# Performance work log

Measured on AMD Instinct MI355X. Metric: run time of the kernel, lower is better.

## Reference

```python
import jax, jax.numpy as jnp
import numpy as np

B, N, D = 2, 2048, 1024
H = 16
DH = D // H
WINDOW = 64
SCALE = 1.0 / np.sqrt(DH).astype(np.float32)


def setup_inputs() -> dict:
    key = jax.random.key(0)
    k1, k2, k3 = jax.random.split(key, 3)
    # xavier-uniform-like scales for the projections
    lim_qkv = np.sqrt(6.0 / (D + 3 * D)).astype(np.float32)
    lim_out = np.sqrt(6.0 / (D + D)).astype(np.float32)
    x = jax.random.normal(k1, (B, N, D), dtype=jnp.float32)
    Wqkv = jax.random.uniform(k2, (3 * D, D), dtype=jnp.float32, minval=-lim_qkv, maxval=lim_qkv)
    bqkv = jnp.zeros((3 * D,), dtype=jnp.float32)
    Wout = jax.random.uniform(k3, (D, D), dtype=jnp.float32, minval=-lim_out, maxval=lim_out)
    bout = jnp.zeros((D,), dtype=jnp.float32)
    return {"x": x, "Wqkv": Wqkv, "bqkv": bqkv, "Wout": Wout, "bout": bout}


def _causal_window_mask(n: int) -> jnp.ndarray:
    pos = jnp.arange(n)
    diff = pos[:, None] - pos[None, :]  # query_pos - key_pos
    return (diff >= 0) & (diff < WINDOW)  # [N, N] bool


def reference(x, Wqkv, bqkv, Wout, bout):
    b, n, d = x.shape
    qkv = x @ Wqkv.T + bqkv                      # [B, N, 3D]
    qkv = qkv.reshape(b, n, 3, H, DH)
    qkv = jnp.transpose(qkv, (2, 0, 3, 1, 4))    # [3, B, H, N, DH]
    q, k, v = qkv[0], qkv[1], qkv[2]
    scores = jnp.einsum('bhqd,bhkd->bhqk', q, k) * SCALE  # [B, H, N, N]
    mask = _causal_window_mask(n)
    neg_inf = jnp.asarray(-jnp.inf, dtype=scores.dtype)
    scores = jnp.where(mask[None, None], scores, neg_inf)
    attn = jax.nn.softmax(scores, axis=-1)
    out = jnp.einsum('bhqk,bhkd->bhqd', attn, v)  # [B, H, N, DH]
    out = jnp.transpose(out, (0, 2, 1, 3)).reshape(b, n, d)
    return out @ Wout.T + bout
```

## Files before the change

### kernel.cpp

```cpp
#include <hip/hip_runtime.h>
#include <hip/hip_bf16.h>


typedef __attribute__((ext_vector_type(8))) __bf16 bf16x8;
typedef __attribute__((ext_vector_type(4))) float f32x4;

#define GLOAD16(g, l)                                              \
  __builtin_amdgcn_global_load_lds(                                \
      (const __attribute__((address_space(1))) void*)(g),          \
      (__attribute__((address_space(3))) void*)(l), 16, 0, 0)

#define MFMA16(a, b, c) __builtin_amdgcn_mfma_f32_16x16x32_bf16((a), (b), (c), 0, 0, 0)

__global__ __launch_bounds__(256) void cvt3(const float* __restrict__ x,
                                            const float* __restrict__ wqkv,
                                            const float* __restrict__ wout,
                                            __bf16* __restrict__ xb,
                                            __bf16* __restrict__ wqkvb,
                                            __bf16* __restrict__ woutb) {
  const int blk = blockIdx.x;
  const float* src;
  __bf16* dst;
  int i;
  if (blk < 2048) {
    src = x; dst = xb; i = (blk * 256 + (int)threadIdx.x) * 8;
  } else if (blk < 3584) {
    src = wqkv; dst = wqkvb; i = ((blk - 2048) * 256 + (int)threadIdx.x) * 8;
  } else {
    src = wout; dst = woutb; i = ((blk - 3584) * 256 + (int)threadIdx.x) * 8;
  }
  f32x4 a = *(const f32x4*)(src + i);
  f32x4 b = *(const f32x4*)(src + i + 4);
  bf16x8 o;
  o[0] = (__bf16)a[0]; o[1] = (__bf16)a[1]; o[2] = (__bf16)a[2]; o[3] = (__bf16)a[3];
  o[4] = (__bf16)b[0]; o[5] = (__bf16)b[1]; o[6] = (__bf16)b[2]; o[7] = (__bf16)b[3];
  *(bf16x8*)(dst + i) = o;
}

template <int MODE, int WM>
__global__ __launch_bounds__(WM * 128) void gemm_ct(
    const __bf16* __restrict__ A, const __bf16* __restrict__ Bw,
    const float* __restrict__ bias, int N,
    float* __restrict__ outF,
    __bf16* __restrict__ qo, __bf16* __restrict__ ko, __bf16* __restrict__ vt,
    int nbn, int chunk) {
  constexpr int K = 1024;
  constexpr int ASZ = WM * 8192;
  constexpr int BUF = ASZ + 16384;
  __shared__ __align__(16) unsigned char Ls[2 * BUF];
  const int tid = threadIdx.x;
  const int lane = tid & 63;
  const int wid = tid >> 6;
  const int wr = (WM == 2) ? (wid >> 1) : 0;
  const int wc = (WM == 2) ? (wid & 1) : wid;
  const int colL = lane & 15, g = lane >> 4;

  int s = (int)blockIdx.x;
  s = (s & 7) * chunk + (s >> 3);
  const int m0 = (s / nbn) * (WM * 64), n0 = (s % nbn) * 128;

  const __bf16* Ap = A + (size_t)m0 * K;
  const __bf16* Bp = Bw + (size_t)n0 * K;

  auto stageA = [&](unsigned char* lds, int k0) {
#pragma unroll
    for (int it = 0; it < 4; ++it) {
      int c = tid + it * (WM * 128);
      int row = c >> 3, p = c & 7, q = p ^ (row & 7);
      GLOAD16(Ap + (size_t)row * K + k0 + (q << 3), lds + c * 16);
    }
  };
  auto stageB = [&](unsigned char* lds, int k0) {
#pragma unroll
    for (int it = 0; it < 8 / WM; ++it) {
      int c = tid + it * (WM * 128);
      int row = c >> 3, p = c & 7, q = p ^ (row & 7);
      GLOAD16(Bp + (size_t)row * K + k0 + (q << 3), lds + c * 16);
    }
  };

  f32x4 acc[4][4] = {};

  stageA(Ls, 0);
  stageB(Ls + ASZ, 0);
  stageA(Ls + BUF, 64);
  stageB(Ls + BUF + ASZ, 64);
  if constexpr (WM == 2) asm volatile("s_waitcnt vmcnt(8)" ::: "memory");
  else                   asm volatile("s_waitcnt vmcnt(12)" ::: "memory");
  __builtin_amdgcn_s_barrier();

  constexpr int nT = 16;
  for (int t = 0; t < nT; ++t) {
    const unsigned char* Ab = Ls + (t & 1) * BUF;
    const unsigned char* Bb = Ab + ASZ;
    bf16x8 af[4][2], bf[4][2];
#pragma unroll
    for (int mi = 0; mi < 4; ++mi) {
      const int r = (wr << 6) + (mi << 4) + colL;
#pragma unroll
      for (int kk = 0; kk < 2; ++kk)
        af[mi][kk] = *(const bf16x8*)(Ab + r * 128 + ((((kk << 2) + g) ^ (r & 7)) << 4));
    }
#pragma unroll
    for (int ni = 0; ni < 4; ++ni) {
      const int r = (wc << 6) + (ni << 4) + colL;
#pragma unroll
      for (int kk = 0; kk < 2; ++kk)
        bf[ni][kk] = *(const bf16x8*)(Bb + r * 128 + ((((kk << 2) + g) ^ (r & 7)) << 4));
    }
#pragma unroll
    for (int mi = 0; mi < 4; ++mi)
#pragma unroll
      for (int ni = 0; ni < 4; ++ni) {
        acc[mi][ni] = MFMA16(af[mi][0], bf[ni][0], acc[mi][ni]);
        acc[mi][ni] = MFMA16(af[mi][1], bf[ni][1], acc[mi][ni]);
      }
    asm volatile("s_waitcnt lgkmcnt(0)" ::: "memory");
    __builtin_amdgcn_s_barrier();
    if (t < nT - 2) {
      const int kn = (t + 2) << 6;
      unsigned char* dst = Ls + (t & 1) * BUF;
      stageA(dst, kn);
      stageB(dst + ASZ, kn);
      if constexpr (WM == 2) asm volatile("s_waitcnt vmcnt(8)" ::: "memory");
      else                   asm volatile("s_waitcnt vmcnt(12)" ::: "memory");
    } else {
      asm volatile("s_waitcnt vmcnt(0)" ::: "memory");
    }
    __builtin_amdgcn_s_barrier();
  }

  if (MODE == 0) {
    const int Cn0 = n0 + (wc << 6);
    const int sx = Cn0 >> 10, h = (Cn0 >> 6) & 15;
    float bv[4];
#pragma unroll
    for (int ni = 0; ni < 4; ++ni) bv[ni] = bias[Cn0 + (ni << 4) + colL];
    const int b = m0 >> 11;
    if (sx == 2) {
      unsigned char* wreg = Ls + wid * 9216;
#pragma unroll
      for (int mi = 0; mi < 4; ++mi)
#pragma unroll
        for (int ni = 0; ni < 4; ++ni)
#pragma unroll
          for (int jp = 0; jp < 2; ++jp) {
            const int tt = (mi << 4) + (g << 2) + (jp << 1);
            const int d = (ni << 4) + colL;
            unsigned short u0 = __builtin_bit_cast(
                unsigned short, (__bf16)(acc[mi][ni][jp * 2] + bv[ni]));
            unsigned short u1 = __builtin_bit_cast(
                unsigned short, (__bf16)(acc[mi][ni][jp * 2 + 1] + bv[ni]));
            *(unsigned int*)(wreg + ((d * 72 + tt) << 1)) =
                (unsigned int)u0 | ((unsigned int)u1 << 16);
          }
      asm volatile("s_waitcnt lgkmcnt(0)" ::: "memory");
      const size_t vbase = (size_t)(b * 16 + h) * 64 * 2048;
      const int tg0 = (m0 & 2047) + (wr << 6);
#pragma unroll
      for (int i = 0; i < 32; ++i) {
        const int d = (i << 1) + (lane >> 5);
        const int toff = (lane & 31) << 1;
        unsigned int v = *(unsigned int*)(wreg + (d * 144 + ((lane & 31) << 2)));
        *(unsigned int*)((unsigned short*)vt + vbase + (size_t)d * 2048 + tg0 + toff) = v;
      }
    } else {
      __bf16* dst = (sx == 0) ? qo : ko;
      const float mul = (sx == 0) ? 0.125f : 1.0f;
#pragma unroll
      for (int mi = 0; mi < 4; ++mi) {
#pragma unroll
        for (int j = 0; j < 4; ++j) {
          const int Rm = m0 + (wr << 6) + (mi << 4) + (g << 2) + j;
          const int tt = Rm & 2047;
          __bf16* rowp = dst + (((size_t)b * 16 + h) * 2048 + tt) * 64;
#pragma unroll
          for (int ni = 0; ni < 4; ++ni)
            rowp[(ni << 4) + colL] = (__bf16)((acc[mi][ni][j] + bv[ni]) * mul);
        }
      }
    }
  } else {
    float bv[4];
#pragma unroll
    for (int ni = 0; ni < 4; ++ni) bv[ni] = bias[n0 + (wc << 6) + (ni << 4) + colL];
#pragma unroll
    for (int mi = 0; mi < 4; ++mi) {
#pragma unroll
      for (int j = 0; j < 4; ++j) {
        const int Rm = m0 + (wr << 6) + (mi << 4) + (g << 2) + j;
        float* rowp = outF + (size_t)Rm * N + n0 + (wc << 6);
#pragma unroll
        for (int ni = 0; ni < 4; ++ni)
          rowp[(ni << 4) + colL] = acc[mi][ni][j] + bv[ni];
      }
    }
  }
}

__global__ __launch_bounds__(256) void attn_win(const __bf16* __restrict__ Qb,
                                                const __bf16* __restrict__ Kb,
                                                const __bf16* __restrict__ Vt,
                                                __bf16* __restrict__ Ob) {
  const int bh = blockIdx.x >> 5;
  const int qb = blockIdx.x & 31;
  const int b = bh >> 4, h = bh & 15;
  __shared__ __align__(16) unsigned char Qs[64 * 128];
  __shared__ __align__(16) unsigned char Ks[128 * 128];
  __shared__ __align__(16) unsigned char Vs[64 * 256];
  __shared__ __align__(16) unsigned char Ps[4 * 16 * 272];
  const int tid = threadIdx.x;
  const int lane = tid & 63;
  const int w = tid >> 6;
  const int colL = lane & 15, g = lane >> 4;
  const __bf16* Qg = Qb + (size_t)bh * 2048 * 64;
  const __bf16* Kg = Kb + (size_t)bh * 2048 * 64;
  const __bf16* Vg = Vt + (size_t)bh * 64 * 2048;
  const int t0 = qb * 64 - 64;

#pragma unroll
  for (int it = 0; it < 2; ++it) {
    int c = tid + (it << 8);
    int r = c >> 3, p = c & 7, q = p ^ (r & 7);
    GLOAD16(Qg + (size_t)(qb * 64 + r) * 64 + (q << 3), Qs + c * 16);
  }
#pragma unroll
  for (int it = 0; it < 4; ++it) {
    int c = tid + (it << 8);
    int r = c >> 3, p = c & 7, q = p ^ (r & 7);
    int tok = t0 + r;
    tok = tok < 0 ? 0 : tok;
    GLOAD16(Kg + (size_t)tok * 64 + (q << 3), Ks + c * 16);
  }
#pragma unroll
  for (int it = 0; it < 4; ++it) {
    int c = tid + (it << 8);
    int r = c >> 4, p = c & 15, q = p ^ (r & 7);
    int tk = t0 + (q << 3);
    tk = tk < 0 ? 0 : tk;
    GLOAD16(Vg + (size_t)r * 2048 + tk, Vs + c * 16);
  }
  __syncthreads();

  f32x4 sc[8] = {};
  bf16x8 qf[2];
#pragma unroll
  for (int kk = 0; kk < 2; ++kk) {
    int r = (w << 4) + colL;
    int slot = (kk << 2) + g;
    qf[kk] = *(const bf16x8*)(Qs + r * 128 + ((slot ^ (r & 7)) << 4));
  }
#pragma unroll
  for (int ni = 0; ni < 8; ++ni) {
#pragma unroll
    for (int kk = 0; kk < 2; ++kk) {
      int r = (ni << 4) + colL;
      int slot = (kk << 2) + g;
      bf16x8 kf = *(const bf16x8*)(Ks + r * 128 + ((slot ^ (r & 7)) << 4));
      sc[ni] = MFMA16(qf[kk], kf, sc[ni]);
    }
  }

  float mx[4], sm[4];
#pragma unroll
  for (int j = 0; j < 4; ++j) mx[j] = -3.0e38f;
#pragma unroll
  for (int ni = 0; ni < 8; ++ni) {
#pragma unroll
    for (int j = 0; j < 4; ++j) {
      const int qi = (w << 4) + (g << 2) + j;
      const int ki = (ni << 4) + colL;
      const bool valid = (ki > qi) && (ki <= qi + 64) && (qb > 0 || ki >= 64);
      if (!valid) sc[ni][j] = -3.0e38f;
      mx[j] = fmaxf(mx[j], sc[ni][j]);
    }
  }
#pragma unroll
  for (int j = 0; j < 4; ++j) {
    mx[j] = fmaxf(mx[j], __shfl_xor(mx[j], 1));
    mx[j] = fmaxf(mx[j], __shfl_xor(mx[j], 2));
    mx[j] = fmaxf(mx[j], __shfl_xor(mx[j], 4));
    mx[j] = fmaxf(mx[j], __shfl_xor(mx[j], 8));
    sm[j] = 0.0f;
  }
  unsigned char* ps = Ps + w * (16 * 272);
#pragma unroll
  for (int ni = 0; ni < 8; ++ni) {
#pragma unroll
    for (int j = 0; j < 4; ++j) {
      float p = __expf(sc[ni][j] - mx[j]);
      sm[j] += p;
      *(__bf16*)(ps + ((g << 2) + j) * 272 + (((ni << 4) + colL) << 1)) = (__bf16)p;
    }
  }
#pragma unroll
  for (int j = 0; j < 4; ++j) {
    sm[j] += __shfl_xor(sm[j], 1);
    sm[j] += __shfl_xor(sm[j], 2);
    sm[j] += __shfl_xor(sm[j], 4);
    sm[j] += __shfl_xor(sm[j], 8);
  }
  __syncthreads();

  f32x4 o[4] = {};
#pragma unroll
  for (int step = 0; step < 4; ++step) {
    bf16x8 pf = *(const bf16x8*)(ps + colL * 272 + (step << 6) + (g << 4));
#pragma unroll
    for (int dt = 0; dt < 4; ++dt) {
      int r = (dt << 4) + colL;
      int slot = (step << 2) + g;
      bf16x8 vf = *(const bf16x8*)(Vs + r * 256 + ((slot ^ (r & 7)) << 4));
      o[dt] = MFMA16(pf, vf, o[dt]);
    }
  }

  float rinv[4];
#pragma unroll
  for (int j = 0; j < 4; ++j) rinv[j] = 1.0f / sm[j];
#pragma unroll
  for (int dt = 0; dt < 4; ++dt) {
#pragma unroll
    for (int j = 0; j < 4; ++j) {
      const int t = qb * 64 + (w << 4) + (g << 2) + j;
      Ob[((size_t)b * 2048 + t) * 1024 + h * 64 + (dt << 4) + colL] =
          (__bf16)(o[dt][j] * rinv[j]);
    }
  }
}

extern "C" void kernel_launch(void* const* d_in, const int* in_sizes, int n_in,
                              void* d_out, int out_size, void* d_ws, size_t ws_size,
                              hipStream_t stream) {
  const float* x = (const float*)d_in[0];
  const float* Wqkv = (const float*)d_in[1];
  const float* bqkv = (const float*)d_in[2];
  const float* Wout = (const float*)d_in[3];
  const float* bout = (const float*)d_in[4];
  float* out = (float*)d_out;

  __bf16* xb = (__bf16*)d_ws;
  __bf16* Wqkvb = xb + 4194304;
  __bf16* Woutb = Wqkvb + 3145728;
  __bf16* Qb = Woutb + 1048576;
  __bf16* Kb = Qb + 4194304;
  __bf16* Vtb = Kb + 4194304;
  __bf16* AOb = Vtb + 4194304;

  cvt3<<<4096, 256, 0, stream>>>(x, Wqkv, Wout, xb, Wqkvb, Woutb);
  gemm_ct<0, 2><<<768, 256, 0, stream>>>(xb, Wqkvb, bqkv, 3072, nullptr,
                                         Qb, Kb, Vtb, 24, 96);
  attn_win<<<1024, 256, 0, stream>>>(Qb, Kb, Vtb, AOb);
  gemm_ct<1, 1><<<512, 128, 0, stream>>>(AOb, Woutb, bout, 1024, out,
                                         nullptr, nullptr, nullptr, 8, 64);
}
```

Measured before the change: 72.87 us.

## Specialize QKV GEMM with K=32 double-buffered tiles and precomputed LDS addresses

```diff
diff --git a/kernel.cpp b/kernel.cpp
--- a/kernel.cpp
+++ b/kernel.cpp
@@ -37,27 +37,158 @@
   *(bf16x8*)(dst + i) = o;
 }
 
-template <int MODE, int WM>
-__global__ __launch_bounds__(WM * 128) void gemm_ct(
+__global__ __launch_bounds__(256) void gemm_qkv(
+    const __bf16* __restrict__ A, const __bf16* __restrict__ Bw,
+    const float* __restrict__ bias,
+    __bf16* __restrict__ qo, __bf16* __restrict__ ko, __bf16* __restrict__ vt) {
+  constexpr int K = 1024;
+  __shared__ __align__(16) unsigned char Ls[36864];
+  const int tid = threadIdx.x;
+  const int lane = tid & 63;
+  const int wid = tid >> 6;
+  const int wr = wid >> 1, wc = wid & 1;
+  const int colL = lane & 15, g = lane >> 4;
+
+  int s = (int)blockIdx.x;
+  s = (s & 7) * 96 + (s >> 3);
+  const int m0 = (s / 24) * 128, n0 = (s % 24) * 128;
+
+  const __bf16* Ap = A + (size_t)m0 * K;
+  const __bf16* Bp = Bw + (size_t)n0 * K;
+
+  const int c0 = tid, c1 = tid + 256;
+  auto srcoff = [&](int c) {
+    int L = c >> 3, s6 = c & 7, u = s6 ^ (L & 7);
+    int row = (L << 1) | (u >> 2), p = u & 3;
+    return (size_t)row * K + (p << 3);
+  };
+  const size_t soA0 = srcoff(c0), soA1 = srcoff(c1);
+  const int dA0 = c0 * 16, dA1 = c1 * 16;
+  const int dB0 = 8192 + c0 * 16, dB1 = 8192 + c1 * 16;
+
+  const __bf16* pA0 = Ap + soA0 + 64;
+  const __bf16* pA1 = Ap + soA1 + 64;
+  const __bf16* pB0 = Bp + soA0 + 64;
+  const __bf16* pB1 = Bp + soA1 + 64;
+
+  int adrA[4], adrB[4];
+#pragma unroll
+  for (int mi = 0; mi < 4; ++mi) {
+    const int r = (wr << 6) + (mi << 4) + colL;
+    adrA[mi] = (r >> 1) * 128 + (((((r & 1) << 2) | g) ^ ((r >> 1) & 7)) << 4);
+    const int rn = (wc << 6) + (mi << 4) + colL;
+    adrB[mi] = 8192 + (rn >> 1) * 128 + (((((rn & 1) << 2) | g) ^ ((rn >> 1) & 7)) << 4);
+  }
+
+  f32x4 acc[4][4] = {};
+
+  GLOAD16(Ap + soA0, Ls + dA0);
+  GLOAD16(Ap + soA1, Ls + dA1);
+  GLOAD16(Bp + soA0, Ls + dB0);
+  GLOAD16(Bp + soA1, Ls + dB1);
+  GLOAD16(Ap + soA0 + 32, Ls + 16384 + dA0);
+  GLOAD16(Ap + soA1 + 32, Ls + 16384 + dA1);
+  GLOAD16(Bp + soA0 + 32, Ls + 16384 + dB0);
+  GLOAD16(Bp + soA1 + 32, Ls + 16384 + dB1);
+  asm volatile("s_waitcnt vmcnt(4)" ::: "memory");
+  __builtin_amdgcn_s_barrier();
+
+  for (int t = 0; t < 32; ++t) {
+    const int po = (t & 1) << 14;
+    const unsigned char* base = Ls + po;
+    bf16x8 af[4], bf[4];
+#pragma unroll
+    for (int mi = 0; mi < 4; ++mi) af[mi] = *(const bf16x8*)(base + adrA[mi]);
+#pragma unroll
+    for (int ni = 0; ni < 4; ++ni) bf[ni] = *(const bf16x8*)(base + adrB[ni]);
+#pragma unroll
+    for (int mi = 0; mi < 4; ++mi)
+#pragma unroll
+      for (int ni = 0; ni < 4; ++ni)
+        acc[mi][ni] = MFMA16(af[mi], bf[ni], acc[mi][ni]);
+    asm volatile("s_waitcnt lgkmcnt(0)" ::: "memory");
+    __builtin_amdgcn_s_barrier();
+    if (t < 30) {
+      unsigned char* d = Ls + po;
+      GLOAD16(pA0, d + dA0);
+      GLOAD16(pA1, d + dA1);
+      GLOAD16(pB0, d + dB0);
+      GLOAD16(pB1, d + dB1);
+      pA0 += 32; pA1 += 32; pB0 += 32; pB1 += 32;
+      asm volatile("s_waitcnt vmcnt(4)" ::: "memory");
+    } else {
+      asm volatile("s_waitcnt vmcnt(0)" ::: "memory");
+    }
+    __builtin_amdgcn_s_barrier();
+  }
+
+  const int Cn0 = n0 + (wc << 6);
+  const int sx = Cn0 >> 10, h = (Cn0 >> 6) & 15;
+  float bv[4];
+#pragma unroll
+  for (int ni = 0; ni < 4; ++ni) bv[ni] = bias[Cn0 + (ni << 4) + colL];
+  const int b = m0 >> 11;
+  if (sx == 2) {
+    unsigned char* wreg = Ls + wid * 9216;
+#pragma unroll
+    for (int mi = 0; mi < 4; ++mi)
+#pragma unroll
+      for (int ni = 0; ni < 4; ++ni)
+#pragma unroll
+        for (int jp = 0; jp < 2; ++jp) {
+          const int tt = (mi << 4) + (g << 2) + (jp << 1);
+          const int d = (ni << 4) + colL;
+          unsigned short u0 = __builtin_bit_cast(
+              unsigned short, (__bf16)(acc[mi][ni][jp * 2] + bv[ni]));
+          unsigned short u1 = __builtin_bit_cast(
+              unsigned short, (__bf16)(acc[mi][ni][jp * 2 + 1] + bv[ni]));
+          *(unsigned int*)(wreg + ((d * 72 + tt) << 1)) =
+              (unsigned int)u0 | ((unsigned int)u1 << 16);
+        }
+    asm volatile("s_waitcnt lgkmcnt(0)" ::: "memory");
+    const size_t vbase = (size_t)(b * 16 + h) * 64 * 2048;
+    const int tg0 = (m0 & 2047) + (wr << 6);
+#pragma unroll
+    for (int i = 0; i < 32; ++i) {
+      const int d = (i << 1) + (lane >> 5);
+      const int toff = (lane & 31) << 1;
+      unsigned int v = *(unsigned int*)(wreg + (d * 144 + ((lane & 31) << 2)));
+      *(unsigned int*)((unsigned short*)vt + vbase + (size_t)d * 2048 + tg0 + toff) = v;
+    }
+  } else {
+    __bf16* dst = (sx == 0) ? qo : ko;
+    const float mul = (sx == 0) ? 0.125f : 1.0f;
+#pragma unroll
+    for (int mi = 0; mi < 4; ++mi) {
+#pragma unroll
+      for (int j = 0; j < 4; ++j) {
+        const int Rm = m0 + (wr << 6) + (mi << 4) + (g << 2) + j;
+        const int tt = Rm & 2047;
+        __bf16* rowp = dst + (((size_t)b * 16 + h) * 2048 + tt) * 64;
+#pragma unroll
+        for (int ni = 0; ni < 4; ++ni)
+          rowp[(ni << 4) + colL] = (__bf16)((acc[mi][ni][j] + bv[ni]) * mul);
+      }
+    }
+  }
+}
+
+__global__ __launch_bounds__(128) void gemm_out(
     const __bf16* __restrict__ A, const __bf16* __restrict__ Bw,
     const float* __restrict__ bias, int N,
-    float* __restrict__ outF,
-    __bf16* __restrict__ qo, __bf16* __restrict__ ko, __bf16* __restrict__ vt,
-    int nbn, int chunk) {
+    float* __restrict__ outF, int nbn, int chunk) {
   constexpr int K = 1024;
-  constexpr int ASZ = WM * 8192;
+  constexpr int ASZ = 8192;
   constexpr int BUF = ASZ + 16384;
   __shared__ __align__(16) unsigned char Ls[2 * BUF];
   const int tid = threadIdx.x;
   const int lane = tid & 63;
-  const int wid = tid >> 6;
-  const int wr = (WM == 2) ? (wid >> 1) : 0;
-  const int wc = (WM == 2) ? (wid & 1) : wid;
+  const int wc = tid >> 6;
   const int colL = lane & 15, g = lane >> 4;
 
   int s = (int)blockIdx.x;
   s = (s & 7) * chunk + (s >> 3);
-  const int m0 = (s / nbn) * (WM * 64), n0 = (s % nbn) * 128;
+  const int m0 = (s / nbn) * 64, n0 = (s % nbn) * 128;
 
   const __bf16* Ap = A + (size_t)m0 * K;
   const __bf16* Bp = Bw + (size_t)n0 * K;
@@ -65,15 +196,15 @@
   auto stageA = [&](unsigned char* lds, int k0) {
 #pragma unroll
     for (int it = 0; it < 4; ++it) {
-      int c = tid + it * (WM * 128);
+      int c = tid + it * 128;
       int row = c >> 3, p = c & 7, q = p ^ (row & 7);
       GLOAD16(Ap + (size_t)row * K + k0 + (q << 3), lds + c * 16);
     }
   };
   auto stageB = [&](unsigned char* lds, int k0) {
 #pragma unroll
-    for (int it = 0; it < 8 / WM; ++it) {
-      int c = tid + it * (WM * 128);
+    for (int it = 0; it < 8; ++it) {
+      int c = tid + it * 128;
       int row = c >> 3, p = c & 7, q = p ^ (row & 7);
       GLOAD16(Bp + (size_t)row * K + k0 + (q << 3), lds + c * 16);
     }
@@ -85,8 +216,7 @@
   stageB(Ls + ASZ, 0);
   stageA(Ls + BUF, 64);
   stageB(Ls + BUF + ASZ, 64);
-  if constexpr (WM == 2) asm volatile("s_waitcnt vmcnt(8)" ::: "memory");
-  else                   asm volatile("s_waitcnt vmcnt(12)" ::: "memory");
+  asm volatile("s_waitcnt vmcnt(12)" ::: "memory");
   __builtin_amdgcn_s_barrier();
 
   constexpr int nT = 16;
@@ -96,7 +226,7 @@
     bf16x8 af[4][2], bf[4][2];
 #pragma unroll
     for (int mi = 0; mi < 4; ++mi) {
-      const int r = (wr << 6) + (mi << 4) + colL;
+      const int r = (mi << 4) + colL;
 #pragma unroll
       for (int kk = 0; kk < 2; ++kk)
         af[mi][kk] = *(const bf16x8*)(Ab + r * 128 + ((((kk << 2) + g) ^ (r & 7)) << 4));
@@ -122,78 +252,25 @@
       unsigned char* dst = Ls + (t & 1) * BUF;
       stageA(dst, kn);
       stageB(dst + ASZ, kn);
-      if constexpr (WM == 2) asm volatile("s_waitcnt vmcnt(8)" ::: "memory");
-      else                   asm volatile("s_waitcnt vmcnt(12)" ::: "memory");
+      asm volatile("s_waitcnt vmcnt(12)" ::: "memory");
     } else {
       asm volatile("s_waitcnt vmcnt(0)" ::: "memory");
     }
     __builtin_amdgcn_s_barrier();
   }
 
-  if (MODE == 0) {
-    const int Cn0 = n0 + (wc << 6);
-    const int sx = Cn0 >> 10, h = (Cn0 >> 6) & 15;
-    float bv[4];
-#pragma unroll
-    for (int ni = 0; ni < 4; ++ni) bv[ni] = bias[Cn0 + (ni << 4) + colL];
-    const int b = m0 >> 11;
-    if (sx == 2) {
-      unsigned char* wreg = Ls + wid * 9216;
-#pragma unroll
-      for (int mi = 0; mi < 4; ++mi)
-#pragma unroll
-        for (int ni = 0; ni < 4; ++ni)
-#pragma unroll
-          for (int jp = 0; jp < 2; ++jp) {
-            const int tt = (mi << 4) + (g << 2) + (jp << 1);
-            const int d = (ni << 4) + colL;
-            unsigned short u0 = __builtin_bit_cast(
-                unsigned short, (__bf16)(acc[mi][ni][jp * 2] + bv[ni]));
-            unsigned short u1 = __builtin_bit_cast(
-                unsigned short, (__bf16)(acc[mi][ni][jp * 2 + 1] + bv[ni]));
-            *(unsigned int*)(wreg + ((d * 72 + tt) << 1)) =
-                (unsigned int)u0 | ((unsigned int)u1 << 16);
-          }
-      asm volatile("s_waitcnt lgkmcnt(0)" ::: "memory");
-      const size_t vbase = (size_t)(b * 16 + h) * 64 * 2048;
-      const int tg0 = (m0 & 2047) + (wr << 6);
-#pragma unroll
-      for (int i = 0; i < 32; ++i) {
-        const int d = (i << 1) + (lane >> 5);
-        const int toff = (lane & 31) << 1;
-        unsigned int v = *(unsigned int*)(wreg + (d * 144 + ((lane & 31) << 2)));
-        *(unsigned int*)((unsigned short*)vt + vbase + (size_t)d * 2048 + tg0 + toff) = v;
-      }
-    } else {
-      __bf16* dst = (sx == 0) ? qo : ko;
-      const float mul = (sx == 0) ? 0.125f : 1.0f;
-#pragma unroll
-      for (int mi = 0; mi < 4; ++mi) {
-#pragma unroll
-        for (int j = 0; j < 4; ++j) {
-          const int Rm = m0 + (wr << 6) + (mi << 4) + (g << 2) + j;
-          const int tt = Rm & 2047;
-          __bf16* rowp = dst + (((size_t)b * 16 + h) * 2048 + tt) * 64;
-#pragma unroll
-          for (int ni = 0; ni < 4; ++ni)
-            rowp[(ni << 4) + colL] = (__bf16)((acc[mi][ni][j] + bv[ni]) * mul);
-        }
-      }
-    }
-  } else {
-    float bv[4];
-#pragma unroll
-    for (int ni = 0; ni < 4; ++ni) bv[ni] = bias[n0 + (wc << 6) + (ni << 4) + colL];
-#pragma unroll
-    for (int mi = 0; mi < 4; ++mi) {
-#pragma unroll
-      for (int j = 0; j < 4; ++j) {
-        const int Rm = m0 + (wr << 6) + (mi << 4) + (g << 2) + j;
-        float* rowp = outF + (size_t)Rm * N + n0 + (wc << 6);
-#pragma unroll
-        for (int ni = 0; ni < 4; ++ni)
-          rowp[(ni << 4) + colL] = acc[mi][ni][j] + bv[ni];
-      }
+  float bv[4];
+#pragma unroll
+  for (int ni = 0; ni < 4; ++ni) bv[ni] = bias[n0 + (wc << 6) + (ni << 4) + colL];
+#pragma unroll
+  for (int mi = 0; mi < 4; ++mi) {
+#pragma unroll
+    for (int j = 0; j < 4; ++j) {
+      const int Rm = m0 + (mi << 4) + (g << 2) + j;
+      float* rowp = outF + (size_t)Rm * N + n0 + (wc << 6);
+#pragma unroll
+      for (int ni = 0; ni < 4; ++ni)
+        rowp[(ni << 4) + colL] = acc[mi][ni][j] + bv[ni];
     }
   }
 }
@@ -348,9 +425,7 @@
   __bf16* AOb = Vtb + 4194304;
 
   cvt3<<<4096, 256, 0, stream>>>(x, Wqkv, Wout, xb, Wqkvb, Woutb);
-  gemm_ct<0, 2><<<768, 256, 0, stream>>>(xb, Wqkvb, bqkv, 3072, nullptr,
-                                         Qb, Kb, Vtb, 24, 96);
+  gemm_qkv<<<768, 256, 0, stream>>>(xb, Wqkvb, bqkv, Qb, Kb, Vtb);
   attn_win<<<1024, 256, 0, stream>>>(Qb, Kb, Vtb, AOb);
-  gemm_ct<1, 1><<<512, 128, 0, stream>>>(AOb, Woutb, bout, 1024, out,
-                                         nullptr, nullptr, nullptr, 8, 64);
+  gemm_out<<<512, 128, 0, stream>>>(AOb, Woutb, bout, 1024, out, 8, 64);
 }
```

Measured after the change: 80.00 us. 1.1x slower.
